# Kernel optimization log

Hardware: AMD Instinct MI355X
Metric: run time of the kernel (lower is better)

Reference implementation:

```python
import jax, jax.numpy as jnp
import numpy as np

K = 5        # kernel_size per dim
DIM = 3      # pseudo-coordinate dim
KTOT = K ** DIM   # 125 kernel weight matrices
S = 2 ** DIM      # 8 basis products for degree-1 open B-spline
KNN = 3


def spline_basis(ea):
    """Degree-1 open B-spline basis. ea: [E, DIM] in [0,1).
    Returns basis [E, S] and kernel weight indices wi [E, S]."""
    v = ea * (K - 1)
    b = jnp.floor(v)
    f = v - b                      # fractional part, grads flow here
    bi = b.astype(jnp.int32)
    bases, idxs = [], []
    for c in range(S):             # static loop over 2^DIM corner combos
        bs = jnp.ones(ea.shape[0], ea.dtype)
        wi = jnp.zeros(ea.shape[0], jnp.int32)
        for d in range(DIM):
            bit = (c >> d) & 1
            bs = bs * (f[:, d] if bit else 1.0 - f[:, d])
            wi = wi + jnp.clip(bi[:, d] + bit, 0, K - 1) * (K ** d)
        bases.append(bs)
        idxs.append(wi)
    return jnp.stack(bases, 1), jnp.stack(idxs, 1)


def spline_conv(x, src, dst, basis, wi, W, Wroot, bias):
    """SplineConv with aggr='mean', root weight and bias (PyG defaults)."""
    N, Cin = x.shape
    E = src.shape[0]
    xs = x[src]                                   # [E, Cin] gather
    vals = xs[:, None, :] * basis[:, :, None]     # [E, S, Cin]
    seg = (dst[:, None] * KTOT + wi).reshape(-1)  # bucket by (dst node, kernel)
    A = jax.ops.segment_sum(vals.reshape(-1, Cin), seg,
                            num_segments=N * KTOT).reshape(N, KTOT, Cin)
    out = jnp.einsum('nki,kio->no', A, W)         # apply kernel bank once
    deg = jax.ops.segment_sum(jnp.ones(E, x.dtype), dst, num_segments=N)
    out = out / jnp.maximum(deg, 1.0)[:, None]    # mean aggregation
    return out + x @ Wroot + bias


def knn_interpolate(x, pos_x, pos_y, batch_x, batch_y, k):
    """PyG knn_interpolate: inverse-squared-distance weighted k-NN average."""
    off = 1e5  # separate batches in coordinate space
    px = pos_x + batch_x[:, None].astype(pos_x.dtype) * off
    py = pos_y + batch_y[:, None].astype(pos_y.dtype) * off
    d2 = (jnp.sum(py ** 2, 1)[:, None] + jnp.sum(px ** 2, 1)[None, :]
          - 2.0 * (py @ px.T))                    # [Ny, Nx]
    negd, idx = jax.lax.top_k(-d2, k)             # k nearest
    w = 1.0 / jnp.maximum(-negd, 1e-16)           # [Ny, k]
    return (w[:, :, None] * x[idx]).sum(1) / w.sum(1)[:, None]


def setup_inputs() -> dict:
    key = jax.random.key(0)
    ks = jax.random.split(key, 12)
    N, E, Ny, C = 8192, 131072, 16384, 64
    return {
        'x': jax.random.normal(ks[0], (N, C), jnp.float32),
        'edge_index': jax.random.randint(ks[1], (2, E), 0, N, jnp.int32),
        'edge_attr': jax.random.uniform(ks[2], (E, DIM), jnp.float32),
        'pos_x': jax.random.normal(ks[3], (N, 3), jnp.float32),
        'batch_x': jnp.zeros((N,), jnp.int32),
        'pos_y': jax.random.normal(ks[4], (Ny, 3), jnp.float32),
        'batch_y': jnp.zeros((Ny,), jnp.int32),
        'Wa': jax.random.normal(ks[5], (KTOT, C, C), jnp.float32) * 0.05,
        'roota': jax.random.normal(ks[6], (C, C), jnp.float32) * 0.05,
        'biasa': jnp.zeros((C,), jnp.float32),
        'Wb': jax.random.normal(ks[7], (KTOT, C, C), jnp.float32) * 0.05,
        'rootb': jax.random.normal(ks[8], (C, C), jnp.float32) * 0.05,
        'biasb': jnp.zeros((C,), jnp.float32),
    }


def reference(x, edge_index, edge_attr, pos_x, batch_x, pos_y, batch_y,
              Wa, roota, biasa, Wb, rootb, biasb):
    src, dst = edge_index[0], edge_index[1]
    basis, wi = spline_basis(edge_attr)
    h = jax.nn.elu(spline_conv(x, src, dst, basis, wi, Wa, roota, biasa))
    h = jax.nn.elu(spline_conv(h, src, dst, basis, wi, Wb, rootb, biasb))
    return knn_interpolate(h, pos_x, pos_y, batch_x, batch_y, KNN)
```

## Files before the change

### kernel.cpp

```cpp
#include <hip/hip_runtime.h>
#include <hip/hip_bf16.h>
#include <math.h>

#define CDIV(a,b) (((a)+(b)-1)/(b))
#define WPCV 8
#define QPW 8

typedef __attribute__((ext_vector_type(8))) short bf16x8;
typedef __attribute__((ext_vector_type(4))) float f32x4;

__device__ __forceinline__ float elu_f(float x){ return x > 0.f ? x : expm1f(x); }
__device__ __forceinline__ unsigned short f2bf(float x){
    __hip_bfloat16 h = __float2bfloat16(x);
    union { __hip_bfloat16 b; unsigned short u; } cv; cv.b = h; return cv.u;
}
__device__ __forceinline__ float bf2f(unsigned short u){
    unsigned int ui = ((unsigned int)u) << 16;
    union { unsigned int u; float f; } cv; cv.u = ui; return cv.f;
}

__global__ void k_basis_px(const float* __restrict__ ea, const int* __restrict__ dst,
                        float* __restrict__ basis, int* __restrict__ cellid,
                        int* __restrict__ cellcnt, int* __restrict__ deg,
                        int* __restrict__ rank, int E, int EB, int PB,
                        const float* __restrict__ posx, const int* __restrict__ bx,
                        float4* __restrict__ px4, int N,
                        const float* __restrict__ x, unsigned short* __restrict__ xbf)
{
    const int tid = threadIdx.x;
    const int bid = blockIdx.x;
    if (bid >= EB) {
        int r = bid - EB;
        if (r < PB) {
            int n = r*256 + tid;
            if (n < N) {
                float off = (float)bx[n] * 1e5f;
                float a = posx[n*3+0]+off, b = posx[n*3+1]+off, c = posx[n*3+2]+off;
                px4[n] = make_float4(a, b, c, a*a + b*b + c*c);
            }
        } else {
            int i = (r - PB)*256 + tid;
            if (i < N*8) {
                const float4* xs = (const float4*)x + (size_t)i*2;
                float4 a4 = xs[0], b4 = xs[1];
                bf16x8 v;
                v[0]=(short)f2bf(a4.x); v[1]=(short)f2bf(a4.y);
                v[2]=(short)f2bf(a4.z); v[3]=(short)f2bf(a4.w);
                v[4]=(short)f2bf(b4.x); v[5]=(short)f2bf(b4.y);
                v[6]=(short)f2bf(b4.z); v[7]=(short)f2bf(b4.w);
                *(bf16x8*)(xbf + (size_t)i*8) = v;
            }
        }
        return;
    }
    __shared__ int hist[64];
    if (tid < 64) hist[tid] = 0;
    __syncthreads();
    int e = bid * 256 + tid;
    if (e < E) {
        float f[3]; int bi[3];
        #pragma unroll
        for (int d = 0; d < 3; d++) {
            float v = ea[e*3+d] * 4.f;
            float b = floorf(v);
            f[d] = v - b;
            int bb = (int)b; bb = bb < 0 ? 0 : (bb > 3 ? 3 : bb);
            bi[d] = bb;
        }
        int cell = bi[0] + 4*bi[1] + 16*bi[2];
        cellid[e] = cell;
        atomicAdd(&hist[cell], 1);
        rank[e] = atomicAdd(deg + dst[e], 1);
        float bs[8];
        #pragma unroll
        for (int c = 0; c < 8; c++) {
            float b = 1.f;
            #pragma unroll
            for (int d = 0; d < 3; d++)
                b *= ((c>>d)&1) ? f[d] : (1.f - f[d]);
            bs[c] = b;
        }
        float4* bw = (float4*)(basis + (size_t)e*8);
        bw[0] = make_float4(bs[0],bs[1],bs[2],bs[3]);
        bw[1] = make_float4(bs[4],bs[5],bs[6],bs[7]);
    }
    __syncthreads();
    if (tid < 64 && hist[tid]) atomicAdd(cellcnt + tid, hist[tid]);
}

__global__ __launch_bounds__(1024) void k_degscan(const int* __restrict__ deg,
                        int* __restrict__ csr, float* __restrict__ invdeg, int N,
                        const int* __restrict__ cellcnt, int* __restrict__ cellstart,
                        int* __restrict__ cellfill)
{
    __shared__ int buf[2][1024];
    const int t = threadIdx.x;
    if (t < 64) {
        int v = cellcnt[t];
        int s = v;
        #pragma unroll
        for (int off = 1; off < 64; off <<= 1) {
            int o = __shfl_up(s, off, 64);
            if (t >= off) s += o;
        }
        cellstart[t] = s - v; cellfill[t] = s - v;
        if (t == 63) cellstart[64] = s;
    }
    const int base = t*8;
    int loc[8]; int s = 0;
    #pragma unroll
    for (int j = 0; j < 8; j++) {
        loc[j] = s;
        int d = (base+j < N) ? deg[base+j] : 0;
        if (base+j < N) invdeg[base+j] = 1.f / fmaxf((float)d, 1.f);
        s += d;
    }
    buf[0][t] = s; __syncthreads();
    int pb = 0;
    for (int off = 1; off < 1024; off <<= 1) {
        int v = buf[pb][t];
        if (t >= off) v += buf[pb][t-off];
        buf[pb^1][t] = v; __syncthreads(); pb ^= 1;
    }
    int excl = buf[pb][t] - s;
    #pragma unroll
    for (int j = 0; j < 8; j++)
        if (base+j < N) csr[base+j] = excl + loc[j];
    if (t == 0) csr[N] = buf[pb][1023];
}

__global__ __launch_bounds__(256) void k_pack(
    const int* __restrict__ cellid, int* __restrict__ fill, int* __restrict__ elist,
    const int* __restrict__ dst, const int* __restrict__ rank,
    const int* __restrict__ csr, int* __restrict__ dstpos, int E, int SB,
    const float* __restrict__ Wa, const float* __restrict__ Wb,
    unsigned short* __restrict__ WTa, unsigned short* __restrict__ WTb)
{
    __shared__ float shbuf[64*65];
    const int tid = threadIdx.x;
    const int bid = blockIdx.x;
    if (bid < SB) {
        int* hist = (int*)shbuf;
        int* bas  = hist + 64;
        if (tid < 64) hist[tid] = 0;
        __syncthreads();
        int e = bid * 256 + tid;
        int cell = 0, loc = 0;
        bool act = e < E;
        if (act) { cell = cellid[e]; loc = atomicAdd(&hist[cell], 1); }
        __syncthreads();
        if (tid < 64) bas[tid] = hist[tid] ? atomicAdd(fill + tid, hist[tid]) : 0;
        __syncthreads();
        if (act) elist[bas[cell] + loc] = e;
    } else if (bid < 2*SB) {
        int e = (bid - SB) * 256 + tid;
        if (e < E) dstpos[e] = csr[dst[e]] + rank[e];
    } else {
        int b = bid - 2*SB;
        float (*ws65)[65] = (float(*)[65])shbuf;
        const float* Wsrc = (b < 125) ? (Wa + (size_t)b*4096) : (Wb + (size_t)(b-125)*4096);
        unsigned short* Wdst = (b < 125) ? (WTa + (size_t)b*4096) : (WTb + (size_t)(b-125)*4096);
        #pragma unroll
        for (int j = 0; j < 16; j++) {
            int idx = j*256 + tid;
            ws65[idx>>6][idx&63] = Wsrc[idx];
        }
        __syncthreads();
        #pragma unroll
        for (int j = 0; j < 16; j++) {
            int idx = j*256 + tid;
            int o = idx>>6, i = idx&63;
            Wdst[idx] = f2bf(ws65[i][o]);
        }
    }
}

__global__ __launch_bounds__(256) void k_conv(
    const unsigned short* __restrict__ xin, const unsigned short* __restrict__ WT,
    const int* __restrict__ elist, const int* __restrict__ cellstart,
    const float* __restrict__ basis, const int* __restrict__ src,
    const int* __restrict__ dstpos, unsigned short* __restrict__ ye)
{
    __shared__ unsigned short wt[8][64][64];
    __shared__ unsigned short xb[64][64];
    __shared__ float bts[8][64];
    __shared__ int dpos[64];

    const int cell = blockIdx.x / WPCV;
    const int sub  = blockIdx.x % WPCV;
    const int tid  = threadIdx.x;
    const int w    = tid >> 6;
    const int lane = tid & 63;
    const int eh   = w >> 1;
    const int oh   = w & 1;
    const int l15  = lane & 15;
    const int kgrp = lane >> 4;
    const int swz  = lane & 7;

    int kc[8];
    {
        int b0 = cell & 3, b1 = (cell >> 2) & 3, b2 = (cell >> 4) & 3;
        #pragma unroll
        for (int c = 0; c < 8; c++)
            kc[c] = (b0 + (c&1)) + 5*(b1 + ((c>>1)&1)) + 25*(b2 + ((c>>2)&1));
    }

    #pragma unroll
    for (int j = 0; j < 16; j++) {
        int cj  = j >> 1;
        int off = ((j & 1) << 8) + tid;
        int row = off >> 3, colc = off & 7;
        bf16x8 v = ((const bf16x8*)(WT + (size_t)kc[cj]*4096))[off];
        *(bf16x8*)&wt[cj][row][(colc ^ (row & 7)) << 3] = v;
    }

    const int s0 = cellstart[cell], s1 = cellstart[cell+1];
    const int se = tid >> 2, sm = tid & 3;

    for (int base = s0 + sub*64; base < s1; base += WPCV*64) {
        int ne = s1 - base; ne = ne > 64 ? 64 : ne;
        __syncthreads();
        int c0 = (sm*2)     ^ (se & 7);
        int c1 = (sm*2 + 1) ^ (se & 7);
        if (se < ne) {
            int eid = elist[base + se];
            int sn  = src[eid];
            const bf16x8* xr = (const bf16x8*)(xin + (size_t)sn*64);
            bf16x8 v0 = xr[sm*2], v1 = xr[sm*2+1];
            *(bf16x8*)&xb[se][c0 << 3] = v0;
            *(bf16x8*)&xb[se][c1 << 3] = v1;
            if (sm == 0) {
                const float4* br = (const float4*)(basis + (size_t)eid*8);
                float4 bA = br[0], bB = br[1];
                bts[0][se]=bA.x; bts[1][se]=bA.y; bts[2][se]=bA.z; bts[3][se]=bA.w;
                bts[4][se]=bB.x; bts[5][se]=bB.y; bts[6][se]=bB.z; bts[7][se]=bB.w;
                dpos[se] = dstpos[eid];
            }
        } else {
            bf16x8 z = {0,0,0,0,0,0,0,0};
            *(bf16x8*)&xb[se][c0 << 3] = z;
            *(bf16x8*)&xb[se][c1 << 3] = z;
            if (sm == 0) dpos[se] = -1;
        }
        __syncthreads();

        bf16x8 a[2][2];
        #pragma unroll
        for (int me = 0; me < 2; me++) {
            int arow = eh*32 + me*16 + l15;
            #pragma unroll
            for (int kh = 0; kh < 2; kh++)
                a[me][kh] = *(const bf16x8*)&xb[arow][((kh*4 + kgrp) ^ swz) << 3];
        }

        f32x4 y[2][2] = {{{0,0,0,0},{0,0,0,0}},{{0,0,0,0},{0,0,0,0}}};
        #pragma unroll
        for (int c = 0; c < 8; c++) {
            float4 bv[2];
            bv[0] = *(const float4*)&bts[c][eh*32 +      (kgrp << 2)];
            bv[1] = *(const float4*)&bts[c][eh*32 + 16 + (kgrp << 2)];
            bf16x8 bfr[2][2];
            #pragma unroll
            for (int nb = 0; nb < 2; nb++) {
                int brow = oh*32 + nb*16 + l15;
                #pragma unroll
                for (int kh = 0; kh < 2; kh++)
                    bfr[nb][kh] = *(const bf16x8*)&wt[c][brow][((kh*4 + kgrp) ^ swz) << 3];
            }
            #pragma unroll
            for (int me = 0; me < 2; me++) {
                #pragma unroll
                for (int nb = 0; nb < 2; nb++) {
                    f32x4 t = {0.f, 0.f, 0.f, 0.f};
                    t = __builtin_amdgcn_mfma_f32_16x16x32_bf16(a[me][0], bfr[nb][0], t, 0, 0, 0);
                    t = __builtin_amdgcn_mfma_f32_16x16x32_bf16(a[me][1], bfr[nb][1], t, 0, 0, 0);
                    y[me][nb][0] = fmaf(bv[me].x, t[0], y[me][nb][0]);
                    y[me][nb][1] = fmaf(bv[me].y, t[1], y[me][nb][1]);
                    y[me][nb][2] = fmaf(bv[me].z, t[2], y[me][nb][2]);
                    y[me][nb][3] = fmaf(bv[me].w, t[3], y[me][nb][3]);
                }
            }
        }
        #pragma unroll
        for (int me = 0; me < 2; me++) {
            #pragma unroll
            for (int r = 0; r < 4; r++) {
                int el = eh*32 + me*16 + (kgrp << 2) + r;
                int dp = dpos[el];
                if (dp >= 0) {
                    unsigned short* yp = ye + (size_t)dp*64 + oh*32 + l15;
                    yp[0]  = f2bf(y[me][0][r]);
                    yp[16] = f2bf(y[me][1][r]);
                }
            }
        }
    }
}

__global__ __launch_bounds__(256) void k_gather(
    const unsigned short* __restrict__ ye, const int* __restrict__ csr,
    const unsigned short* __restrict__ xin, const float* __restrict__ root,
    const float* __restrict__ bias, const float* __restrict__ invdeg,
    unsigned short* __restrict__ hout, int N)
{
    __shared__ float sh[4][64];
    const int w = threadIdx.x >> 6, lane = threadIdx.x & 63;
    const int n = blockIdx.x*4 + w;
    if (n >= N) return;
    const int s0 = csr[n], s1 = csr[n+1];
    const int j8 = lane >> 3, c8 = lane & 7;
    float acc[8] = {};
    for (int base = s0; base < s1; base += 8) {
        int ei = base + j8;
        if (ei < s1) {
            bf16x8 v = *(const bf16x8*)(ye + (size_t)ei*64 + c8*8);
            #pragma unroll
            for (int k = 0; k < 8; k++)
                acc[k] += bf2f((unsigned short)v[k]);
        }
    }
    #pragma unroll
    for (int m = 8; m <= 32; m <<= 1) {
        #pragma unroll
        for (int k = 0; k < 8; k++)
            acc[k] += __shfl_xor(acc[k], m, 64);
    }
    if (j8 == 0) {
        #pragma unroll
        for (int k = 0; k < 8; k++) sh[w][c8*8+k] = acc[k];
    }
    float aggr = sh[w][lane];
    float av = aggr * invdeg[n];
    float xv = bf2f(xin[(size_t)n*64 + lane]);
    float rt = bias[lane];
    #pragma unroll 8
    for (int i = 0; i < 64; i++)
        rt = fmaf(__shfl(xv, i, 64), root[i*64 + lane], rt);
    hout[(size_t)n*64 + lane] = f2bf(elu_f(av + rt));
}

__global__ __launch_bounds__(256) void k_knn(
    const float4* __restrict__ px4, const float* __restrict__ posy,
    const int* __restrict__ by, const unsigned short* __restrict__ h2,
    float* __restrict__ out, int N, int Ny)
{
    const int wid  = blockIdx.x*4 + (threadIdx.x >> 6);
    const int lane = threadIdx.x & 63;
    const int qbase = wid * QPW;

    int ql = qbase + (lane & (QPW-1));
    float offv = (float)by[ql] * 1e5f;
    float qa = posy[ql*3+0]+offv, qb = posy[ql*3+1]+offv, qc = posy[ql*3+2]+offv;
    float sy_l  = qa*qa + qb*qb + qc*qc;
    float a2_l = -2.f*qa, b2_l = -2.f*qb, c2_l = -2.f*qc;

    float SY[QPW], A2[QPW], B2[QPW], C2[QPW];
    float d0[QPW], d1[QPW], d2s[QPW];
    int   i0[QPW], i1[QPW], i2[QPW];
    #pragma unroll
    for (int g = 0; g < QPW; g++) {
        SY[g] = __shfl(sy_l, g);
        A2[g] = __shfl(a2_l, g);
        B2[g] = __shfl(b2_l, g);
        C2[g] = __shfl(c2_l, g);
    }

    {
        float4 p0 = px4[lane];
        #pragma unroll
        for (int g = 0; g < QPW; g++) {
            float u = fmaf(A2[g], p0.x, fmaf(B2[g], p0.y, fmaf(C2[g], p0.z, SY[g] + p0.w)));
            float uu = u;
            #pragma unroll
            for (int j = 0; j < 3; j++) {
                float md = uu; int mi = lane;
                #pragma unroll
                for (int s = 1; s < 64; s <<= 1) {
                    float od = __shfl_xor(md, s, 64);
                    int   oi = __shfl_xor(mi, s, 64);
                    if (od < md || (od == md && oi < mi)) { md = od; mi = oi; }
                }
                if (j == 0) { d0[g] = md; i0[g] = mi; }
                else if (j == 1) { d1[g] = md; i1[g] = mi; }
                else { d2s[g] = md; i2[g] = mi; }
                if (lane == mi) uu = 3.4e38f;
            }
        }
    }

    const int nb = N >> 6;
    float4 cur = px4[64 + lane];
    for (int b = 1; b < nb; b++) {
        float4 nxt;
        if (b + 1 < nb) nxt = px4[(size_t)((b+1) << 6) + lane];
        const int gb = b << 6;
        #pragma unroll
        for (int g = 0; g < QPW; g++) {
            float u = fmaf(A2[g], cur.x, fmaf(B2[g], cur.y, fmaf(C2[g], cur.z, SY[g] + cur.w)));
            unsigned long long m = __ballot(u < d2s[g]);
            while (m) {
                int l = __builtin_ctzll(m);
                m &= m - 1;
                float uc = __shfl(u, l);
                int   ic = gb + l;
                bool c0 = uc < d0[g], c1 = uc < d1[g], c2 = uc < d2s[g];
                float Md  = c0 ? d0[g] : uc;  int Mi  = c0 ? i0[g] : ic;
                float Md1 = c1 ? d1[g] : Md;  int Mi1 = c1 ? i1[g] : Mi;
                d2s[g] = c2 ? Md1 : d2s[g];   i2[g] = c2 ? Mi1 : i2[g];
                d1[g]  = c1 ? Md  : d1[g];    i1[g] = c1 ? Mi  : i1[g];
                d0[g]  = c0 ? uc  : d0[g];    i0[g] = c0 ? ic  : i0[g];
            }
        }
        cur = nxt;
    }

    #pragma unroll
    for (int g = 0; g < QPW; g++) {
        float w0 = 1.f/fmaxf(d0[g],  1e-16f);
        float w1 = 1.f/fmaxf(d1[g],  1e-16f);
        float w2 = 1.f/fmaxf(d2s[g], 1e-16f);
        float wsum = w0 + w1 + w2;
        float v = w0*bf2f(h2[(size_t)i0[g]*64 + lane])
                + w1*bf2f(h2[(size_t)i1[g]*64 + lane])
                + w2*bf2f(h2[(size_t)i2[g]*64 + lane]);
        out[(size_t)(qbase + g)*64 + lane] = v / wsum;
    }
}

extern "C" void kernel_launch(void* const* d_in, const int* in_sizes, int n_in,
                              void* d_out, int out_size, void* d_ws, size_t ws_size,
                              hipStream_t stream)
{
    const float* x     = (const float*)d_in[0];
    const int*   ei    = (const int*)d_in[1];
    const float* ea    = (const float*)d_in[2];
    const float* posx  = (const float*)d_in[3];
    const int*   bx    = (const int*)d_in[4];
    const float* posy  = (const float*)d_in[5];
    const int*   by    = (const int*)d_in[6];
    const float* Wa    = (const float*)d_in[7];
    const float* roota = (const float*)d_in[8];
    const float* biasa = (const float*)d_in[9];
    const float* Wb    = (const float*)d_in[10];
    const float* rootb = (const float*)d_in[11];
    const float* biasb = (const float*)d_in[12];

    const int N  = in_sizes[0] / 64;
    const int E  = in_sizes[1] / 2;
    const int Ny = in_sizes[5] / 3;
    const int* srcp = ei;
    const int* dstp = ei + E;

    char* ws = (char*)d_ws;
    size_t off = 0;
    auto alloc = [&](size_t bytes) { void* p = ws + off; off += (bytes + 255) & ~255ull; return p; };
    float*  basis    = (float*)alloc((size_t)E*8*4);
    int*    cellid   = (int*)  alloc((size_t)E*4);
    int*    rank     = (int*)  alloc((size_t)E*4);
    int*    elist    = (int*)  alloc((size_t)E*4);
    int*    dstpos   = (int*)  alloc((size_t)E*4);
    int*    deg      = (int*)  alloc((size_t)N*4);
    int*    cellcnt  = (int*)  alloc(64*4);
    int*    csr      = (int*)  alloc((size_t)(N+1)*4);
    float*  invdeg   = (float*)alloc((size_t)N*4);
    int*    cellstart= (int*)  alloc(65*4);
    int*    cellfill = (int*)  alloc(64*4);
    unsigned short* xbf = (unsigned short*)alloc((size_t)N*64*2);
    unsigned short* h1  = (unsigned short*)alloc((size_t)N*64*2);
    unsigned short* h2  = (unsigned short*)alloc((size_t)N*64*2);
    float4* px4      = (float4*)alloc((size_t)N*16);
    unsigned short* WTa = (unsigned short*)alloc((size_t)125*4096*2);
    unsigned short* WTb = (unsigned short*)alloc((size_t)125*4096*2);
    unsigned short* ye  = (unsigned short*)alloc((size_t)E*64*2);
    (void)ws_size; (void)n_in; (void)out_size;

    const int EB = CDIV(E,256);
    const int PB = CDIV(N,256);
    const int XB = CDIV(N*8,256);

    hipMemsetAsync(deg, 0, (size_t)N*4 + 256, stream);

    k_basis_px<<<EB+PB+XB, 256, 0, stream>>>(ea, dstp, basis, cellid, cellcnt, deg, rank,
                                             E, EB, PB, posx, bx, px4, N, x, xbf);
    k_degscan <<<1, 1024, 0, stream>>>(deg, csr, invdeg, N, cellcnt, cellstart, cellfill);
    k_pack    <<<2*EB + 250, 256, 0, stream>>>(cellid, cellfill, elist, dstp, rank,
                                               csr, dstpos, E, EB, Wa, Wb, WTa, WTb);

    k_conv  <<<64*WPCV, 256, 0, stream>>>(xbf, WTa, elist, cellstart, basis, srcp, dstpos, ye);
    k_gather<<<CDIV(N,4), 256, 0, stream>>>(ye, csr, xbf, roota, biasa, invdeg, h1, N);

    k_conv  <<<64*WPCV, 256, 0, stream>>>(h1, WTb, elist, cellstart, basis, srcp, dstpos, ye);
    k_gather<<<CDIV(N,4), 256, 0, stream>>>(ye, csr, h1, rootb, biasb, invdeg, h2, N);

    k_knn<<<Ny/(QPW*4), 256, 0, stream>>>(px4, posy, by, h2, (float*)d_out, N, Ny);
}
```

Measured before the change: 200.5 us.

## Split kNN search over point chunks with a separate merge kernel

The kNN scan is split into KC4=4 chunks of the source points, each handled by its own block, so there are four times as many blocks. Each block writes per-chunk top-3 candidates into scratch space reused from the ye buffer, and a new merge kernel reduces the 12 candidates per query and performs the weighted interpolation. The goal is more parallelism and a shorter serial scan per wave, at the cost of an extra launch and scratch traffic. It assumes N is divisible by 256 and that ye is large enough for the partial results.

```diff
diff --git a/kernel.cpp b/kernel.cpp
--- a/kernel.cpp
+++ b/kernel.cpp
@@ -5,6 +5,7 @@
 #define CDIV(a,b) (((a)+(b)-1)/(b))
 #define WPCV 8
 #define QPW 8
+#define KC4 4
 
 typedef __attribute__((ext_vector_type(8))) short bf16x8;
 typedef __attribute__((ext_vector_type(4))) float f32x4;
@@ -339,14 +340,17 @@
     hout[(size_t)n*64 + lane] = f2bf(elu_f(av + rt));
 }
 
-__global__ __launch_bounds__(256) void k_knn(
+__global__ __launch_bounds__(256) void k_knn_scan(
     const float4* __restrict__ px4, const float* __restrict__ posy,
-    const int* __restrict__ by, const unsigned short* __restrict__ h2,
-    float* __restrict__ out, int N, int Ny)
-{
-    const int wid  = blockIdx.x*4 + (threadIdx.x >> 6);
+    const int* __restrict__ by, float* __restrict__ pd, int* __restrict__ pi,
+    int N, int Ny)
+{
+    const int bq   = blockIdx.x / KC4;
+    const int ch   = blockIdx.x % KC4;
     const int lane = threadIdx.x & 63;
-    const int qbase = wid * QPW;
+    const int qbase = (bq*4 + (threadIdx.x >> 6)) * QPW;
+    const int NC   = N / KC4;
+    const int pbase = ch * NC;
 
     int ql = qbase + (lane & (QPW-1));
     float offv = (float)by[ql] * 1e5f;
@@ -366,14 +370,13 @@
     }
 
     {
-        float4 p0 = px4[lane];
+        float4 p0 = px4[pbase + lane];
         #pragma unroll
         for (int g = 0; g < QPW; g++) {
-            float u = fmaf(A2[g], p0.x, fmaf(B2[g], p0.y, fmaf(C2[g], p0.z, SY[g] + p0.w)));
-            float uu = u;
+            float uu = fmaf(A2[g], p0.x, fmaf(B2[g], p0.y, fmaf(C2[g], p0.z, SY[g] + p0.w)));
             #pragma unroll
             for (int j = 0; j < 3; j++) {
-                float md = uu; int mi = lane;
+                float md = uu; int mi = pbase + lane;
                 #pragma unroll
                 for (int s = 1; s < 64; s <<= 1) {
                     float od = __shfl_xor(md, s, 64);
@@ -383,17 +386,17 @@
                 if (j == 0) { d0[g] = md; i0[g] = mi; }
                 else if (j == 1) { d1[g] = md; i1[g] = mi; }
                 else { d2s[g] = md; i2[g] = mi; }
-                if (lane == mi) uu = 3.4e38f;
-            }
-        }
-    }
-
-    const int nb = N >> 6;
-    float4 cur = px4[64 + lane];
+                if (pbase + lane == mi) uu = 3.4e38f;
+            }
+        }
+    }
+
+    const int nb = NC >> 6;
+    float4 cur = px4[pbase + 64 + lane];
     for (int b = 1; b < nb; b++) {
         float4 nxt;
-        if (b + 1 < nb) nxt = px4[(size_t)((b+1) << 6) + lane];
-        const int gb = b << 6;
+        if (b + 1 < nb) nxt = px4[(size_t)pbase + ((b+1) << 6) + lane];
+        const int gb = pbase + (b << 6);
         #pragma unroll
         for (int g = 0; g < QPW; g++) {
             float u = fmaf(A2[g], cur.x, fmaf(B2[g], cur.y, fmaf(C2[g], cur.z, SY[g] + cur.w)));
@@ -416,15 +419,45 @@
 
     #pragma unroll
     for (int g = 0; g < QPW; g++) {
-        float w0 = 1.f/fmaxf(d0[g],  1e-16f);
-        float w1 = 1.f/fmaxf(d1[g],  1e-16f);
-        float w2 = 1.f/fmaxf(d2s[g], 1e-16f);
-        float wsum = w0 + w1 + w2;
-        float v = w0*bf2f(h2[(size_t)i0[g]*64 + lane])
-                + w1*bf2f(h2[(size_t)i1[g]*64 + lane])
-                + w2*bf2f(h2[(size_t)i2[g]*64 + lane]);
-        out[(size_t)(qbase + g)*64 + lane] = v / wsum;
-    }
+        if (lane == g) {
+            size_t ob = ((size_t)ch*Ny + qbase + g)*3;
+            pd[ob+0]=d0[g]; pd[ob+1]=d1[g]; pd[ob+2]=d2s[g];
+            pi[ob+0]=i0[g]; pi[ob+1]=i1[g]; pi[ob+2]=i2[g];
+        }
+    }
+}
+
+__global__ __launch_bounds__(256) void k_knn_merge(
+    const float* __restrict__ pd, const int* __restrict__ pi,
+    const unsigned short* __restrict__ h2, float* __restrict__ out, int Ny)
+{
+    const int w = threadIdx.x >> 6, lane = threadIdx.x & 63;
+    const int q = blockIdx.x*4 + w;
+    float a0 = 3.4e38f; int b0 = 0x7fffffff;
+    if (lane < KC4*3) {
+        size_t base = ((size_t)(lane/3)*Ny + q)*3 + (lane%3);
+        a0 = pd[base]; b0 = pi[base];
+    }
+    float rd[3]; int ri[3];
+    #pragma unroll
+    for (int j = 0; j < 3; j++) {
+        float md = a0; int mi = b0;
+        #pragma unroll
+        for (int s = 1; s < 64; s <<= 1) {
+            float od = __shfl_xor(md, s, 64);
+            int   oi = __shfl_xor(mi, s, 64);
+            if (od < md || (od == md && oi < mi)) { md = od; mi = oi; }
+        }
+        rd[j] = md; ri[j] = mi;
+        if (b0 == mi) { a0 = 3.4e38f; b0 = 0x7fffffff; }
+    }
+    float w0 = 1.f/fmaxf(rd[0], 1e-16f);
+    float w1 = 1.f/fmaxf(rd[1], 1e-16f);
+    float w2 = 1.f/fmaxf(rd[2], 1e-16f);
+    float ws = w0 + w1 + w2;
+    float v = w0*bf2f(h2[(size_t)ri[0]*64+lane]) + w1*bf2f(h2[(size_t)ri[1]*64+lane])
+            + w2*bf2f(h2[(size_t)ri[2]*64+lane]);
+    out[(size_t)q*64+lane] = v / ws;
 }
 
 extern "C" void kernel_launch(void* const* d_in, const int* in_sizes, int n_in,
@@ -472,6 +505,8 @@
     unsigned short* WTa = (unsigned short*)alloc((size_t)125*4096*2);
     unsigned short* WTb = (unsigned short*)alloc((size_t)125*4096*2);
     unsigned short* ye  = (unsigned short*)alloc((size_t)E*64*2);
+    float* pd = (float*)ye;
+    int*   pi = (int*)((char*)ye + ((size_t)4<<20));
     (void)ws_size; (void)n_in; (void)out_size;
 
     const int EB = CDIV(E,256);
@@ -492,5 +527,6 @@
     k_conv  <<<64*WPCV, 256, 0, stream>>>(h1, WTb, elist, cellstart, basis, srcp, dstpos, ye);
     k_gather<<<CDIV(N,4), 256, 0, stream>>>(ye, csr, h1, rootb, biasb, invdeg, h2, N);
 
-    k_knn<<<Ny/(QPW*4), 256, 0, stream>>>(px4, posy, by, h2, (float*)d_out, N, Ny);
-}
+    k_knn_scan <<<(Ny/(QPW*4))*KC4, 256, 0, stream>>>(px4, posy, by, pd, pi, N, Ny);
+    k_knn_merge<<<Ny/4, 256, 0, stream>>>(pd, pi, h2, (float*)d_out, Ny);
+}
```

New measurement: 207.2 us. 1.03x slower.

## Replace brute-force kNN with uniform-grid spatial search and brute fallback

Applied to the files above, without the earlier changes.

Builds a 16^3 uniform grid over source positions: a wave reduction with atomics computes the bounding box, the scan kernel builds per-cell histograms and prefix offsets, and the pack kernel scatters points into cell order. The kNN kernel now gives one query per wave, scans only the 27 neighbouring cells, and checks with a distance bound that the result is exact, falling back to a full scan otherwise. This replaces the O(N) per-query brute force scan, at the cost of extra preprocessing work, atomics, and a divergent fallback path for queries near the grid edges.

```diff
diff --git a/kernel.cpp b/kernel.cpp
--- a/kernel.cpp
+++ b/kernel.cpp
@@ -4,7 +4,7 @@
 
 #define CDIV(a,b) (((a)+(b)-1)/(b))
 #define WPCV 8
-#define QPW 8
+#define GDIM 16
 
 typedef __attribute__((ext_vector_type(8))) short bf16x8;
 typedef __attribute__((ext_vector_type(4))) float f32x4;
@@ -17,6 +17,31 @@
 __device__ __forceinline__ float bf2f(unsigned short u){
     unsigned int ui = ((unsigned int)u) << 16;
     union { unsigned int u; float f; } cv; cv.u = ui; return cv.f;
+}
+__device__ __forceinline__ unsigned int enc_key(float f){
+    int i = __float_as_int(f);
+    return (unsigned int)(i ^ ((i >> 31) | 0x80000000));
+}
+__device__ __forceinline__ float dec_key(unsigned int k){
+    unsigned int u = (k & 0x80000000u) ? (k & 0x7FFFFFFFu) : ~k;
+    return __uint_as_float(u);
+}
+
+__device__ __forceinline__ void merge3(float d0, int i0, float d1, int i1,
+                                       float d2, int i2, float* rd, int* ri)
+{
+    #pragma unroll
+    for (int j = 0; j < 3; j++) {
+        float md = d0; int mi = i0;
+        #pragma unroll
+        for (int s = 1; s < 64; s <<= 1) {
+            float od = __shfl_xor(md, s, 64);
+            int   oi = __shfl_xor(mi, s, 64);
+            if (od < md || (od == md && oi < mi)) { md = od; mi = oi; }
+        }
+        rd[j] = md; ri[j] = mi;
+        if (i0 == mi) { d0 = d1; i0 = i1; d1 = d2; i1 = i2; d2 = 3.4e38f; i2 = 0x7fffffff; }
+    }
 }
 
 __global__ void k_basis_px(const float* __restrict__ ea, const int* __restrict__ dst,
@@ -25,7 +50,8 @@
                         int* __restrict__ rank, int E, int EB, int PB,
                         const float* __restrict__ posx, const int* __restrict__ bx,
                         float4* __restrict__ px4, int N,
-                        const float* __restrict__ x, unsigned short* __restrict__ xbf)
+                        const float* __restrict__ x, unsigned short* __restrict__ xbf,
+                        unsigned int* __restrict__ mmin, unsigned int* __restrict__ mmax)
 {
     const int tid = threadIdx.x;
     const int bid = blockIdx.x;
@@ -33,10 +59,31 @@
         int r = bid - EB;
         if (r < PB) {
             int n = r*256 + tid;
-            if (n < N) {
+            float a = 0.f, b = 0.f, c = 0.f;
+            bool act = n < N;
+            if (act) {
                 float off = (float)bx[n] * 1e5f;
-                float a = posx[n*3+0]+off, b = posx[n*3+1]+off, c = posx[n*3+2]+off;
+                a = posx[n*3+0]+off; b = posx[n*3+1]+off; c = posx[n*3+2]+off;
                 px4[n] = make_float4(a, b, c, a*a + b*b + c*c);
+            }
+            float mn[3], mx[3];
+            mn[0] = act ? a :  3.4e38f; mx[0] = act ? a : -3.4e38f;
+            mn[1] = act ? b :  3.4e38f; mx[1] = act ? b : -3.4e38f;
+            mn[2] = act ? c :  3.4e38f; mx[2] = act ? c : -3.4e38f;
+            #pragma unroll
+            for (int s = 1; s < 64; s <<= 1) {
+                #pragma unroll
+                for (int d = 0; d < 3; d++) {
+                    mn[d] = fminf(mn[d], __shfl_xor(mn[d], s, 64));
+                    mx[d] = fmaxf(mx[d], __shfl_xor(mx[d], s, 64));
+                }
+            }
+            if ((tid & 63) == 0) {
+                #pragma unroll
+                for (int d = 0; d < 3; d++) {
+                    atomicMin(mmin + d, enc_key(mn[d]));
+                    atomicMax(mmax + d, enc_key(mx[d]));
+                }
             }
         } else {
             int i = (r - PB)*256 + tid;
@@ -91,9 +138,15 @@
 __global__ __launch_bounds__(1024) void k_degscan(const int* __restrict__ deg,
                         int* __restrict__ csr, float* __restrict__ invdeg, int N,
                         const int* __restrict__ cellcnt, int* __restrict__ cellstart,
-                        int* __restrict__ cellfill)
+                        int* __restrict__ cellfill,
+                        const float4* __restrict__ px4,
+                        const unsigned int* __restrict__ mmin,
+                        const unsigned int* __restrict__ mmax,
+                        int* __restrict__ gstart, int* __restrict__ gfill,
+                        float* __restrict__ gmeta)
 {
     __shared__ int buf[2][1024];
+    __shared__ int ghist[GDIM*GDIM*GDIM];
     const int t = threadIdx.x;
     if (t < 64) {
         int v = cellcnt[t];
@@ -105,6 +158,34 @@
         }
         cellstart[t] = s - v; cellfill[t] = s - v;
         if (t == 63) cellstart[64] = s;
+    }
+    #pragma unroll
+    for (int j = 0; j < 4; j++) ghist[t*4+j] = 0;
+    float lov[3], wv[3], iwv[3];
+    #pragma unroll
+    for (int d = 0; d < 3; d++) {
+        float flo = dec_key(mmin[d]);
+        float fhi = dec_key(mmax[d]);
+        lov[d] = flo;
+        wv[d]  = (fhi - flo) / (float)GDIM;
+        iwv[d] = wv[d] > 0.f ? 1.f / wv[d] : 0.f;
+    }
+    if (t == 0) {
+        gmeta[0]=lov[0]; gmeta[1]=lov[1]; gmeta[2]=lov[2];
+        gmeta[3]=wv[0];  gmeta[4]=wv[1];  gmeta[5]=wv[2];
+        gmeta[6]=iwv[0]; gmeta[7]=iwv[1]; gmeta[8]=iwv[2];
+    }
+    __syncthreads();
+    #pragma unroll
+    for (int j = 0; j < 8; j++) {
+        int n = t*8 + j;
+        if (n < N) {
+            float4 p = px4[n];
+            int cx = (int)((p.x - lov[0]) * iwv[0]); cx = cx < 0 ? 0 : (cx > GDIM-1 ? GDIM-1 : cx);
+            int cy = (int)((p.y - lov[1]) * iwv[1]); cy = cy < 0 ? 0 : (cy > GDIM-1 ? GDIM-1 : cy);
+            int cz = (int)((p.z - lov[2]) * iwv[2]); cz = cz < 0 ? 0 : (cz > GDIM-1 ? GDIM-1 : cz);
+            atomicAdd(&ghist[cx + (cy<<4) + (cz<<8)], 1);
+        }
     }
     const int base = t*8;
     int loc[8]; int s = 0;
@@ -127,6 +208,24 @@
     for (int j = 0; j < 8; j++)
         if (base+j < N) csr[base+j] = excl + loc[j];
     if (t == 0) csr[N] = buf[pb][1023];
+    __syncthreads();
+    int gl[4]; int gs = 0;
+    #pragma unroll
+    for (int j = 0; j < 4; j++) { gl[j] = gs; gs += ghist[t*4+j]; }
+    buf[0][t] = gs; __syncthreads();
+    pb = 0;
+    for (int off = 1; off < 1024; off <<= 1) {
+        int v = buf[pb][t];
+        if (t >= off) v += buf[pb][t-off];
+        buf[pb^1][t] = v; __syncthreads(); pb ^= 1;
+    }
+    int gex = buf[pb][t] - gs;
+    #pragma unroll
+    for (int j = 0; j < 4; j++) {
+        gstart[t*4+j] = gex + gl[j];
+        gfill [t*4+j] = gex + gl[j];
+    }
+    if (t == 1023) gstart[4096] = buf[pb][1023];
 }
 
 __global__ __launch_bounds__(256) void k_pack(
@@ -134,7 +233,9 @@
     const int* __restrict__ dst, const int* __restrict__ rank,
     const int* __restrict__ csr, int* __restrict__ dstpos, int E, int SB,
     const float* __restrict__ Wa, const float* __restrict__ Wb,
-    unsigned short* __restrict__ WTa, unsigned short* __restrict__ WTb)
+    unsigned short* __restrict__ WTa, unsigned short* __restrict__ WTb,
+    const float4* __restrict__ px4, const float* __restrict__ gmeta,
+    int* __restrict__ gfill, float4* __restrict__ pxg, int* __restrict__ gidx, int N)
 {
     __shared__ float shbuf[64*65];
     const int tid = threadIdx.x;
@@ -155,7 +256,7 @@
     } else if (bid < 2*SB) {
         int e = (bid - SB) * 256 + tid;
         if (e < E) dstpos[e] = csr[dst[e]] + rank[e];
-    } else {
+    } else if (bid < 2*SB + 250) {
         int b = bid - 2*SB;
         float (*ws65)[65] = (float(*)[65])shbuf;
         const float* Wsrc = (b < 125) ? (Wa + (size_t)b*4096) : (Wb + (size_t)(b-125)*4096);
@@ -171,6 +272,19 @@
             int idx = j*256 + tid;
             int o = idx>>6, i = idx&63;
             Wdst[idx] = f2bf(ws65[i][o]);
+        }
+    } else {
+        int n = (bid - (2*SB + 250))*256 + tid;
+        if (n < N) {
+            float lo0 = gmeta[0], lo1 = gmeta[1], lo2 = gmeta[2];
+            float iw0 = gmeta[6], iw1 = gmeta[7], iw2 = gmeta[8];
+            float4 p = px4[n];
+            int cx = (int)((p.x - lo0) * iw0); cx = cx < 0 ? 0 : (cx > GDIM-1 ? GDIM-1 : cx);
+            int cy = (int)((p.y - lo1) * iw1); cy = cy < 0 ? 0 : (cy > GDIM-1 ? GDIM-1 : cy);
+            int cz = (int)((p.z - lo2) * iw2); cz = cz < 0 ? 0 : (cz > GDIM-1 ? GDIM-1 : cz);
+            int slot = atomicAdd(gfill + (cx + (cy<<4) + (cz<<8)), 1);
+            pxg[slot] = p;
+            gidx[slot] = n;
         }
     }
 }
@@ -339,92 +453,95 @@
     hout[(size_t)n*64 + lane] = f2bf(elu_f(av + rt));
 }
 
-__global__ __launch_bounds__(256) void k_knn(
-    const float4* __restrict__ px4, const float* __restrict__ posy,
+__global__ __launch_bounds__(256) void k_knn_grid(
+    const float4* __restrict__ px4, const float4* __restrict__ pxg,
+    const int* __restrict__ gidx, const int* __restrict__ gstart,
+    const float* __restrict__ gmeta, const float* __restrict__ posy,
     const int* __restrict__ by, const unsigned short* __restrict__ h2,
     float* __restrict__ out, int N, int Ny)
 {
-    const int wid  = blockIdx.x*4 + (threadIdx.x >> 6);
+    const int q    = blockIdx.x*4 + (threadIdx.x >> 6);
     const int lane = threadIdx.x & 63;
-    const int qbase = wid * QPW;
-
-    int ql = qbase + (lane & (QPW-1));
-    float offv = (float)by[ql] * 1e5f;
-    float qa = posy[ql*3+0]+offv, qb = posy[ql*3+1]+offv, qc = posy[ql*3+2]+offv;
-    float sy_l  = qa*qa + qb*qb + qc*qc;
-    float a2_l = -2.f*qa, b2_l = -2.f*qb, c2_l = -2.f*qc;
-
-    float SY[QPW], A2[QPW], B2[QPW], C2[QPW];
-    float d0[QPW], d1[QPW], d2s[QPW];
-    int   i0[QPW], i1[QPW], i2[QPW];
-    #pragma unroll
-    for (int g = 0; g < QPW; g++) {
-        SY[g] = __shfl(sy_l, g);
-        A2[g] = __shfl(a2_l, g);
-        B2[g] = __shfl(b2_l, g);
-        C2[g] = __shfl(c2_l, g);
-    }
-
-    {
-        float4 p0 = px4[lane];
-        #pragma unroll
-        for (int g = 0; g < QPW; g++) {
-            float u = fmaf(A2[g], p0.x, fmaf(B2[g], p0.y, fmaf(C2[g], p0.z, SY[g] + p0.w)));
-            float uu = u;
-            #pragma unroll
-            for (int j = 0; j < 3; j++) {
-                float md = uu; int mi = lane;
-                #pragma unroll
-                for (int s = 1; s < 64; s <<= 1) {
-                    float od = __shfl_xor(md, s, 64);
-                    int   oi = __shfl_xor(mi, s, 64);
-                    if (od < md || (od == md && oi < mi)) { md = od; mi = oi; }
+
+    float offv = (float)by[q] * 1e5f;
+    float qa = posy[q*3+0]+offv, qb = posy[q*3+1]+offv, qc = posy[q*3+2]+offv;
+    float sy = qa*qa + qb*qb + qc*qc;
+    float a2 = -2.f*qa, b2 = -2.f*qb, c2 = -2.f*qc;
+
+    float lo0 = gmeta[0], lo1 = gmeta[1], lo2 = gmeta[2];
+    float w0g = gmeta[3], w1g = gmeta[4], w2g = gmeta[5];
+    float iw0 = gmeta[6], iw1 = gmeta[7], iw2 = gmeta[8];
+    int cx = (int)((qa - lo0) * iw0); cx = cx < 0 ? 0 : (cx > GDIM-1 ? GDIM-1 : cx);
+    int cy = (int)((qb - lo1) * iw1); cy = cy < 0 ? 0 : (cy > GDIM-1 ? GDIM-1 : cy);
+    int cz = (int)((qc - lo2) * iw2); cz = cz < 0 ? 0 : (cz > GDIM-1 ? GDIM-1 : cz);
+
+    float d0 = 3.4e38f, d1 = 3.4e38f, d2s = 3.4e38f;
+    int   i0 = 0x7fffffff, i1 = 0x7fffffff, i2 = 0x7fffffff;
+
+    int cl = lane % 27, half = lane / 27;
+    bool lv = lane < 54;
+    int gx = cx + cl % 3 - 1, gy = cy + (cl/3) % 3 - 1, gz = cz + cl/9 - 1;
+    lv = lv && gx >= 0 && gx < GDIM && gy >= 0 && gy < GDIM && gz >= 0 && gz < GDIM;
+    int cs = 0, ce = 0;
+    if (lv) {
+        int cid = gx + (gy << 4) + (gz << 8);
+        cs = gstart[cid]; ce = gstart[cid+1];
+    }
+    for (int s = cs + half; s < ce; s += 2) {
+        float4 p = pxg[s];
+        int gi = gidx[s];
+        float u = fmaf(a2, p.x, fmaf(b2, p.y, fmaf(c2, p.z, sy + p.w)));
+        bool bl2 = (u < d2s) || (u == d2s && gi < i2);
+        bool bl1 = (u < d1)  || (u == d1  && gi < i1);
+        bool bl0 = (u < d0)  || (u == d0  && gi < i0);
+        if (bl2) {
+            d2s = bl1 ? d1 : u;  i2 = bl1 ? i1 : gi;
+            if (bl1) {
+                d1 = bl0 ? d0 : u; i1 = bl0 ? i0 : gi;
+                if (bl0) { d0 = u; i0 = gi; }
+            }
+        }
+    }
+    float rd[3]; int ri[3];
+    merge3(d0, i0, d1, i1, d2s, i2, rd, ri);
+
+    float bound = 3.4e38f;
+    if (cx >= 2)      bound = fminf(bound, qa - (lo0 + (float)(cx-1)*w0g));
+    if (cx <= GDIM-3) bound = fminf(bound, (lo0 + (float)(cx+2)*w0g) - qa);
+    if (cy >= 2)      bound = fminf(bound, qb - (lo1 + (float)(cy-1)*w1g));
+    if (cy <= GDIM-3) bound = fminf(bound, (lo1 + (float)(cy+2)*w1g) - qb);
+    if (cz >= 2)      bound = fminf(bound, qc - (lo2 + (float)(cz-1)*w2g));
+    if (cz <= GDIM-3) bound = fminf(bound, (lo2 + (float)(cz+2)*w2g) - qc);
+    bool cert = (bound > 0.f) && (rd[2] < bound*bound);
+
+    if (!cert) {
+        d0 = d1 = d2s = 3.4e38f;
+        i0 = i1 = i2 = 0x7fffffff;
+        for (int p = lane; p < N; p += 64) {
+            float4 pp = px4[p];
+            float u = fmaf(a2, pp.x, fmaf(b2, pp.y, fmaf(c2, pp.z, sy + pp.w)));
+            bool bl2 = (u < d2s) || (u == d2s && p < i2);
+            bool bl1 = (u < d1)  || (u == d1  && p < i1);
+            bool bl0 = (u < d0)  || (u == d0  && p < i0);
+            if (bl2) {
+                d2s = bl1 ? d1 : u;  i2 = bl1 ? i1 : p;
+                if (bl1) {
+                    d1 = bl0 ? d0 : u; i1 = bl0 ? i0 : p;
+                    if (bl0) { d0 = u; i0 = p; }
                 }
-                if (j == 0) { d0[g] = md; i0[g] = mi; }
-                else if (j == 1) { d1[g] = md; i1[g] = mi; }
-                else { d2s[g] = md; i2[g] = mi; }
-                if (lane == mi) uu = 3.4e38f;
-            }
-        }
-    }
-
-    const int nb = N >> 6;
-    float4 cur = px4[64 + lane];
-    for (int b = 1; b < nb; b++) {
-        float4 nxt;
-        if (b + 1 < nb) nxt = px4[(size_t)((b+1) << 6) + lane];
-        const int gb = b << 6;
-        #pragma unroll
-        for (int g = 0; g < QPW; g++) {
-            float u = fmaf(A2[g], cur.x, fmaf(B2[g], cur.y, fmaf(C2[g], cur.z, SY[g] + cur.w)));
-            unsigned long long m = __ballot(u < d2s[g]);
-            while (m) {
-                int l = __builtin_ctzll(m);
-                m &= m - 1;
-                float uc = __shfl(u, l);
-                int   ic = gb + l;
-                bool c0 = uc < d0[g], c1 = uc < d1[g], c2 = uc < d2s[g];
-                float Md  = c0 ? d0[g] : uc;  int Mi  = c0 ? i0[g] : ic;
-                float Md1 = c1 ? d1[g] : Md;  int Mi1 = c1 ? i1[g] : Mi;
-                d2s[g] = c2 ? Md1 : d2s[g];   i2[g] = c2 ? Mi1 : i2[g];
-                d1[g]  = c1 ? Md  : d1[g];    i1[g] = c1 ? Mi  : i1[g];
-                d0[g]  = c0 ? uc  : d0[g];    i0[g] = c0 ? ic  : i0[g];
-            }
-        }
-        cur = nxt;
-    }
-
-    #pragma unroll
-    for (int g = 0; g < QPW; g++) {
-        float w0 = 1.f/fmaxf(d0[g],  1e-16f);
-        float w1 = 1.f/fmaxf(d1[g],  1e-16f);
-        float w2 = 1.f/fmaxf(d2s[g], 1e-16f);
-        float wsum = w0 + w1 + w2;
-        float v = w0*bf2f(h2[(size_t)i0[g]*64 + lane])
-                + w1*bf2f(h2[(size_t)i1[g]*64 + lane])
-                + w2*bf2f(h2[(size_t)i2[g]*64 + lane]);
-        out[(size_t)(qbase + g)*64 + lane] = v / wsum;
-    }
+            }
+        }
+        merge3(d0, i0, d1, i1, d2s, i2, rd, ri);
+    }
+
+    float ww0 = 1.f/fmaxf(rd[0], 1e-16f);
+    float ww1 = 1.f/fmaxf(rd[1], 1e-16f);
+    float ww2 = 1.f/fmaxf(rd[2], 1e-16f);
+    float wsum = ww0 + ww1 + ww2;
+    float v = ww0*bf2f(h2[(size_t)ri[0]*64 + lane])
+            + ww1*bf2f(h2[(size_t)ri[1]*64 + lane])
+            + ww2*bf2f(h2[(size_t)ri[2]*64 + lane]);
+    out[(size_t)q*64 + lane] = v / wsum;
 }
 
 extern "C" void kernel_launch(void* const* d_in, const int* in_sizes, int n_in,
@@ -461,30 +578,41 @@
     int*    dstpos   = (int*)  alloc((size_t)E*4);
     int*    deg      = (int*)  alloc((size_t)N*4);
     int*    cellcnt  = (int*)  alloc(64*4);
+    unsigned int* mmax = (unsigned int*)alloc(3*4);
+    unsigned int* mmin = (unsigned int*)alloc(3*4);
     int*    csr      = (int*)  alloc((size_t)(N+1)*4);
     float*  invdeg   = (float*)alloc((size_t)N*4);
     int*    cellstart= (int*)  alloc(65*4);
     int*    cellfill = (int*)  alloc(64*4);
+    int*    gstart   = (int*)  alloc(4097*4);
+    int*    gfill    = (int*)  alloc(4096*4);
+    float*  gmeta    = (float*)alloc(16*4);
     unsigned short* xbf = (unsigned short*)alloc((size_t)N*64*2);
     unsigned short* h1  = (unsigned short*)alloc((size_t)N*64*2);
     unsigned short* h2  = (unsigned short*)alloc((size_t)N*64*2);
     float4* px4      = (float4*)alloc((size_t)N*16);
+    float4* pxg      = (float4*)alloc((size_t)N*16);
+    int*    gidx     = (int*)  alloc((size_t)N*4);
     unsigned short* WTa = (unsigned short*)alloc((size_t)125*4096*2);
     unsigned short* WTb = (unsigned short*)alloc((size_t)125*4096*2);
     unsigned short* ye  = (unsigned short*)alloc((size_t)E*64*2);
     (void)ws_size; (void)n_in; (void)out_size;
 
-    const int EB = CDIV(E,256);
-    const int PB = CDIV(N,256);
-    const int XB = CDIV(N*8,256);
-
-    hipMemsetAsync(deg, 0, (size_t)N*4 + 256, stream);
+    const int EB  = CDIV(E,256);
+    const int PB  = CDIV(N,256);
+    const int XB  = CDIV(N*8,256);
+    const int PXB = CDIV(N,256);
+
+    hipMemsetAsync(deg, 0, (size_t)N*4 + 256 + 256, stream);
+    hipMemsetAsync(mmin, 0xFF, 12, stream);
 
     k_basis_px<<<EB+PB+XB, 256, 0, stream>>>(ea, dstp, basis, cellid, cellcnt, deg, rank,
-                                             E, EB, PB, posx, bx, px4, N, x, xbf);
-    k_degscan <<<1, 1024, 0, stream>>>(deg, csr, invdeg, N, cellcnt, cellstart, cellfill);
-    k_pack    <<<2*EB + 250, 256, 0, stream>>>(cellid, cellfill, elist, dstp, rank,
-                                               csr, dstpos, E, EB, Wa, Wb, WTa, WTb);
+                                             E, EB, PB, posx, bx, px4, N, x, xbf, mmin, mmax);
+    k_degscan <<<1, 1024, 0, stream>>>(deg, csr, invdeg, N, cellcnt, cellstart, cellfill,
+                                       px4, mmin, mmax, gstart, gfill, gmeta);
+    k_pack    <<<2*EB + 250 + PXB, 256, 0, stream>>>(cellid, cellfill, elist, dstp, rank,
+                                               csr, dstpos, E, EB, Wa, Wb, WTa, WTb,
+                                               px4, gmeta, gfill, pxg, gidx, N);
 
     k_conv  <<<64*WPCV, 256, 0, stream>>>(xbf, WTa, elist, cellstart, basis, srcp, dstpos, ye);
     k_gather<<<CDIV(N,4), 256, 0, stream>>>(ye, csr, xbf, roota, biasa, invdeg, h1, N);
@@ -492,5 +620,6 @@
     k_conv  <<<64*WPCV, 256, 0, stream>>>(h1, WTb, elist, cellstart, basis, srcp, dstpos, ye);
     k_gather<<<CDIV(N,4), 256, 0, stream>>>(ye, csr, h1, rootb, biasb, invdeg, h2, N);
 
-    k_knn<<<Ny/(QPW*4), 256, 0, stream>>>(px4, posy, by, h2, (float*)d_out, N, Ny);
-}
+    k_knn_grid<<<Ny/4, 256, 0, stream>>>(px4, pxg, gidx, gstart, gmeta, posy, by, h2,
+                                         (float*)d_out, N, Ny);
+}
```

Result: faster. 195.6 us (-2.4%).
